# Kernel optimization log

Hardware: AMD Instinct MI355X
Metric: run time of the kernel (lower is better)

The kernel has to match this reference:

```python
import jax, jax.numpy as jnp
import numpy as np

N_USERS = 60000
N_ITEMS = 40000
N_NODES = N_USERS + N_ITEMS
N_EDGES = 1_000_000
D = 64
BN_EPS = 1e-3  # tf.layers.batch_normalization default epsilon


def setup_inputs() -> dict:
    key = jax.random.key(0)
    ks = jax.random.split(key, 16)
    s = 1.0 / np.sqrt(D)  # uniform-ish init scale for [D,D] weights
    w = lambda k: (jax.random.uniform(k, (D, D), jnp.float32, -1.0, 1.0) * s)
    return {
        "u_features": jax.random.normal(ks[0], (N_USERS, D), jnp.float32),
        "v_features": jax.random.normal(ks[1], (N_ITEMS, D), jnp.float32),
        "edge_start": jax.random.randint(ks[2], (N_EDGES,), 0, N_NODES, jnp.int32),
        "edge_end": jax.random.randint(ks[3], (N_EDGES,), 0, N_NODES, jnp.int32),
        "Ui1": w(ks[4]), "Uj1": w(ks[5]), "Vi1": w(ks[6]), "Vj1": w(ks[7]),
        "bu1": jnp.zeros((D,), jnp.float32), "bv1": jnp.zeros((D,), jnp.float32),
        "Ui2": w(ks[8]), "Uj2": w(ks[9]), "Vi2": w(ks[10]), "Vj2": w(ks[11]),
        "bu2": jnp.zeros((D,), jnp.float32), "bv2": jnp.zeros((D,), jnp.float32),
        "R": w(ks[12]),
        "gamma1": jnp.ones((D,), jnp.float32), "beta1": jnp.zeros((D,), jnp.float32),
        "gamma2": jnp.ones((D,), jnp.float32), "beta2": jnp.zeros((D,), jnp.float32),
    }


def _stage(x, Ui, Uj, Vi, Vj, bu, bv, e_start, e_end, n_nodes):
    # gate = sigmoid(E_end@(x Vi) + E_start@(x Vj) + bv)   -> edge gather
    gate = jax.nn.sigmoid((x @ Vi)[e_end] + (x @ Vj)[e_start] + bv)  # [E, D]
    msg = gate * (x @ Ui)[e_start]                                    # [E, D]
    # x Uj + E_end.T @ msg + bu   -> scatter-add to destination nodes
    agg = jax.ops.segment_sum(msg, e_end, num_segments=n_nodes)       # [N, D]
    return x @ Uj + agg + bu


def _batchnorm(x, gamma, beta):
    mean = jnp.mean(x, axis=0)
    var = jnp.var(x, axis=0)
    return gamma * (x - mean) * jax.lax.rsqrt(var + BN_EPS) + beta


def reference(u_features, v_features, edge_start, edge_end,
              Ui1, Uj1, Vi1, Vj1, bu1, bv1,
              Ui2, Uj2, Vi2, Vj2, bu2, bv2,
              R, gamma1, beta1, gamma2, beta2):
    num_users = u_features.shape[0]
    x_in = jnp.concatenate([u_features, v_features], axis=0)  # [N, D]
    n = x_in.shape[0]
    x = _stage(x_in, Ui1, Uj1, Vi1, Vj1, bu1, bv1, edge_start, edge_end, n)
    x = jax.nn.relu(_batchnorm(x, gamma1, beta1))
    x = _stage(x, Ui2, Uj2, Vi2, Vj2, bu2, bv2, edge_start, edge_end, n)
    x = _batchnorm(x, gamma2, beta2)
    x = jax.nn.relu(x + x_in @ R)  # residual branch
    return x[:num_users], x[num_users:]
```

## Files before the change

kernel.cpp:

```cpp
#include <hip/hip_runtime.h>
#include <hip/hip_bf16.h>

#define NUSERS 60000
#define NNODES 100000
#define DD 64
#define NGB 1563
#define GMM 782
#define NBUK 196
#define ESB 2048
#define NBH 400
#define NSH 64

typedef __hip_bfloat16 bf16;
using bf16x8 = __attribute__((ext_vector_type(8))) short;
using f32x4  = __attribute__((ext_vector_type(4))) float;

__device__ __forceinline__ float b2f(bf16 x) { return __bfloat162float(x); }
__device__ __forceinline__ bf16 f2b(float x) { return __float2bfloat16(x); }
__device__ __forceinline__ unsigned short fbits(float x) {
    union { bf16 b; unsigned short u; } cv; cv.b = f2b(x); return cv.u;
}
__device__ __forceinline__ float us2f(unsigned short h) {
    union { unsigned u; float f; } t; t.u = (unsigned)h << 16; return t.f;
}
__device__ __forceinline__ float lo_bf16(unsigned w) {
    union { unsigned u; float f; } t; t.u = w << 16; return t.f;
}
__device__ __forceinline__ float hi_bf16(unsigned w) {
    union { unsigned u; float f; } t; t.u = w & 0xFFFF0000u; return t.f;
}
__device__ __forceinline__ float ldf(const void* p, size_t i, int isbf) {
    if (isbf) return b2f(((const bf16*)p)[i]);
    return ((const float*)p)[i];
}
__device__ __forceinline__ unsigned pack2(float a, float b) {
    return (unsigned)fbits(a) | ((unsigned)fbits(b) << 16);
}
__device__ __forceinline__ unsigned pr2(float x0, float x1, float a0, float a1,
                                        float b0, float b1) {
    float t0 = a0 * x0 + b0, t1 = a1 * x1 + b1;
    t0 = t0 > 0.f ? t0 : 0.f;
    t1 = t1 > 0.f ? t1 : 0.f;
    return pack2(t0, t1);
}

__global__ __launch_bounds__(256) void k_bhist(
    const int* __restrict__ ee, const unsigned short* __restrict__ hsn,
    int* __restrict__ flag, int* __restrict__ bh, int E)
{
    __shared__ int h[256];
    int t = threadIdx.x;
    if (blockIdx.x == 0) {
        int cnt = 0;
        for (int i = t; i < 1024; i += 256) {
            int e = (hsn[2 * i] >> 7) & 0xFF;
            cnt += (e >= 100 && e <= 140) ? 1 : 0;
        }
        h[t] = cnt;
        __syncthreads();
        for (int s = 128; s > 0; s >>= 1) {
            if (t < s) h[t] += h[t + s];
            __syncthreads();
        }
        if (t == 0) flag[0] = (h[0] > 512) ? 1 : 0;
        __syncthreads();
    }
    h[t] = 0;
    __syncthreads();
    for (int e = blockIdx.x * 256 + t; e < E; e += gridDim.x * 256)
        atomicAdd(&h[ee[e] >> 9], 1);
    __syncthreads();
    bh[blockIdx.x * 256 + t] = h[t];
}

__global__ __launch_bounds__(1024) void k_bscan(
    const int* __restrict__ bh, int* __restrict__ bbase,
    int* __restrict__ bcursor, float* __restrict__ redz)
{
    __shared__ int ps[1024];
    __shared__ int sd[256];
    int t = threadIdx.x;
    int col = t & 255, seg = t >> 8;
    int v = 0;
#pragma unroll 4
    for (int b = seg * 100; b < (seg + 1) * 100; b++)
        v += bh[b * 256 + col];
    ps[t] = v;
    __syncthreads();
    int vv = 0;
    if (t < 256) {
        vv = ps[t] + ps[t + 256] + ps[t + 512] + ps[t + 768];
        sd[t] = vv;
    }
    __syncthreads();
    for (int off = 1; off < 256; off <<= 1) {
        int x = (t >= off && t < 256) ? sd[t - off] : 0;
        __syncthreads();
        if (t < 256) sd[t] += x;
        __syncthreads();
    }
    if (t < 256) {
        int excl = sd[t] - vv;
        bbase[t] = excl;
        bcursor[t] = excl;
    }
    for (int i = t; i < 2 * NSH * 256; i += 1024) redz[i] = 0.f;
}

__global__ __launch_bounds__(256) void k_bscatter(
    const int* __restrict__ es, const int* __restrict__ ee,
    int* __restrict__ bcursor, unsigned* __restrict__ ebuf, int E)
{
    __shared__ int h[256], gb[256], lr[256];
    int t = threadIdx.x;
    h[t] = 0;
    lr[t] = 0;
    __syncthreads();
    int base = blockIdx.x * ESB;
    unsigned ent[8];
    int bk[8];
#pragma unroll
    for (int i = 0; i < 8; i++) {
        int e = base + t + i * 256;
        if (e < E) {
            int s = es[e], d = ee[e];
            bk[i] = d >> 9;
            ent[i] = (unsigned)s | ((unsigned)(d & 511) << 20);
            atomicAdd(&h[bk[i]], 1);
        } else bk[i] = -1;
    }
    __syncthreads();
    if (h[t]) gb[t] = atomicAdd(&bcursor[t], h[t]);
    __syncthreads();
#pragma unroll
    for (int i = 0; i < 8; i++) {
        if (bk[i] >= 0) {
            int r = atomicAdd(&lr[bk[i]], 1);
            ebuf[gb[bk[i]] + r] = ent[i];
        }
    }
}

__global__ __launch_bounds__(256) void k_group(
    const int* __restrict__ bbase, const unsigned* __restrict__ ebuf,
    int* __restrict__ rowptr, int* __restrict__ srcidx)
{
    __shared__ int h[512], sc[512];
    int b = blockIdx.x, t = threadIdx.x;
    int lo = bbase[b], hi = bbase[b + 1];
    h[t] = 0;
    h[t + 256] = 0;
    __syncthreads();
    for (int i = lo + t; i < hi; i += 256)
        atomicAdd(&h[ebuf[i] >> 20], 1);
    __syncthreads();
    sc[t] = h[t];
    sc[t + 256] = h[t + 256];
    __syncthreads();
    for (int off = 1; off < 512; off <<= 1) {
        int v0 = (t >= off) ? sc[t - off] : 0;
        int v1 = (t + 256 >= off) ? sc[t + 256 - off] : 0;
        __syncthreads();
        sc[t] += v0;
        sc[t + 256] += v1;
        __syncthreads();
    }
    int n0 = b * 512 + t, n1 = b * 512 + t + 256;
    int e0 = lo + sc[t] - h[t];
    int e1 = lo + sc[t + 256] - h[t + 256];
    if (n0 < NNODES) rowptr[n0] = e0;
    if (n1 < NNODES) rowptr[n1] = e1;
    if (b == NBUK - 1 && t == 0) rowptr[NNODES] = hi;
    h[t] = e0;
    h[t + 256] = e1;
    __syncthreads();
    for (int i = lo + t; i < hi; i += 256) {
        unsigned en = ebuf[i];
        int pos = atomicAdd(&h[en >> 20], 1);
        int s = (int)(en & 0xFFFFF);
        srcidx[pos] = s < NNODES ? s : 0;
    }
}

template <int MODE>
__device__ __forceinline__ void stage_load(
    int tile, int tid, int bfflag,
    const void* u, const void* v, const unsigned short* Aacc,
    const float* ab, uint4& w0, uint4& w1)
{
    int r = tid >> 2, c0 = (tid & 3) * 16;
    int row = tile * DD + r;
    int rowc = row < NNODES ? row : NNODES - 1;
    if (MODE == 0) {
        const void* src = (rowc < NUSERS) ? u : v;
        size_t off = (rowc < NUSERS) ? ((size_t)rowc * DD + c0)
                                     : ((size_t)(rowc - NUSERS) * DD + c0);
        if (bfflag) {
            const uint4* p = (const uint4*)((const unsigned short*)src + off);
            w0 = p[0];
            w1 = p[1];
        } else {
            const float4* p = (const float4*)((const float*)src + off);
            float4 f0 = p[0], f1 = p[1], f2 = p[2], f3 = p[3];
            w0 = make_uint4(pack2(f0.x, f0.y), pack2(f0.z, f0.w),
                            pack2(f1.x, f1.y), pack2(f1.z, f1.w));
            w1 = make_uint4(pack2(f2.x, f2.y), pack2(f2.z, f2.w),
                            pack2(f3.x, f3.y), pack2(f3.z, f3.w));
        }
    } else {
        const uint4* p = (const uint4*)(Aacc + (size_t)rowc * DD + c0);
        unsigned aw[8];
        *(uint4*)&aw[0] = p[0];
        *(uint4*)&aw[4] = p[1];
        const float4* pa = (const float4*)(ab + c0);
        const float4* pb = (const float4*)(ab + 64 + c0);
        float av[16], bv[16];
#pragma unroll
        for (int j = 0; j < 4; j++) {
            float4 fa = pa[j], fb = pb[j];
            av[4 * j] = fa.x; av[4 * j + 1] = fa.y;
            av[4 * j + 2] = fa.z; av[4 * j + 3] = fa.w;
            bv[4 * j] = fb.x; bv[4 * j + 1] = fb.y;
            bv[4 * j + 2] = fb.z; bv[4 * j + 3] = fb.w;
        }
        unsigned ow[8];
#pragma unroll
        for (int j = 0; j < 8; j++)
            ow[j] = pr2(lo_bf16(aw[j]), hi_bf16(aw[j]),
                        av[2 * j], av[2 * j + 1], bv[2 * j], bv[2 * j + 1]);
        w0 = *(uint4*)&ow[0];
        w1 = *(uint4*)&ow[4];
    }
}

__device__ __forceinline__ void stage_store(unsigned short* xbuf, int tid,
                                            const uint4& w0, const uint4& w1)
{
    int r = tid >> 2, c0 = (tid & 3) * 16;
    *(uint4*)&xbuf[r * 72 + c0] = w0;
    *((uint4*)&xbuf[r * 72 + c0] + 1) = w1;
}

template <int MODE>
__global__ __launch_bounds__(256, 4) void k_mm4_mfma(
    const void* __restrict__ u, const void* __restrict__ v,
    const float* __restrict__ red, const void* __restrict__ gm,
    const void* __restrict__ bt,
    const void* __restrict__ W0, const void* __restrict__ W1,
    const void* __restrict__ W2, const void* __restrict__ W3,
    const void* __restrict__ b0, const void* __restrict__ b1,
    const int* __restrict__ flag,
    unsigned short* __restrict__ A, unsigned short* __restrict__ Ed,
    unsigned* __restrict__ Tw)
{
    __shared__ __align__(16) unsigned short lsd[4 * DD * 72];
    __shared__ __align__(16) float abs_s[128];
    const int bfflag = flag[0];
    const int tid = threadIdx.x;

    if (MODE == 1) {
        if (tid < 64) {
            float sm = 0.f, sq = 0.f;
#pragma unroll 8
            for (int s = 0; s < NSH; s++) {
                sm += red[s * 256 + tid];
                sq += red[s * 256 + 128 + tid];
            }
            float mean = sm * (1.f / NNODES);
            float var = sq * (1.f / NNODES) - mean * mean;
            float a = ldf(gm, tid, bfflag) * rsqrtf(var + 1e-3f);
            abs_s[tid] = a;
            abs_s[64 + tid] = ldf(bt, tid, bfflag) - mean * a;
        }
        __syncthreads();
    }

    int t = blockIdx.x;
    uint4 xa, xb;
    stage_load<MODE>(t, tid, bfflag, u, v, A, abs_s, xa, xb);

    if (bfflag) {
#define WSTG_BF(m, src)                                                   \
        _Pragma("unroll")                                                 \
        for (int j = 0; j < 2; j++) {                                     \
            int i = tid + j * 256; int e0 = i * 8;                        \
            *(uint4*)&lsd[(m) * 4608 + (e0 >> 6) * 72 + (e0 & 63)] =      \
                ((const uint4*)(src))[i];                                 \
        }
        WSTG_BF(0, W0) WSTG_BF(1, W1) WSTG_BF(2, W2) WSTG_BF(3, W3)
    } else {
#define WSTG_F32(m, src)                                                  \
        _Pragma("unroll")                                                 \
        for (int j = 0; j < 4; j++) {                                     \
            int i = tid + j * 256; int e0 = i * 4;                        \
            float4 f = ((const float4*)(src))[i];                         \
            *(uint2*)&lsd[(m) * 4608 + (e0 >> 6) * 72 + (e0 & 63)] =      \
                make_uint2(pack2(f.x, f.y), pack2(f.z, f.w));             \
        }
        WSTG_F32(0, W0) WSTG_F32(1, W1) WSTG_F32(2, W2) WSTG_F32(3, W3)
    }
    __syncthreads();

    const int wv = tid >> 6, lane = tid & 63;
    const int quad = lane >> 4, ln = lane & 15;
    const int mA = (wv < 2) ? wv : 2;
    bf16x8 bfrA[2][4], bfrB[2][4];
#pragma unroll
    for (int ks = 0; ks < 2; ks++)
#pragma unroll
        for (int nt = 0; nt < 4; nt++)
#pragma unroll
            for (int j = 0; j < 8; j++)
                bfrA[ks][nt][j] = (short)lsd[mA * 4608 +
                    (ks * 32 + quad * 8 + j) * 72 + nt * 16 + ln];
    if (wv >= 2) {
#pragma unroll
        for (int ks = 0; ks < 2; ks++)
#pragma unroll
            for (int nt = 0; nt < 4; nt++)
#pragma unroll
                for (int j = 0; j < 8; j++)
                    bfrB[ks][nt][j] = (short)lsd[3 * 4608 +
                        (ks * 32 + quad * 8 + j) * 72 + nt * 16 + ln];
    }
    float bias[4];
#pragma unroll
    for (int nt = 0; nt < 4; nt++)
        bias[nt] = (wv == 0) ? ldf(b0, nt * 16 + ln, bfflag)
                 : (wv == 1) ? ldf(b1, nt * 16 + ln, bfflag) : 0.f;
    __syncthreads();

    auto compute = [&](const unsigned short* xt, int row0) {
        if (wv < 2) {
            unsigned short* stg = lsd + (2 + wv) * 4608;
#pragma unroll
            for (int rt = 0; rt < 4; rt++) {
                int m = rt * 16 + ln;
                bf16x8 af0 = *(const bf16x8*)&xt[m * 72 + quad * 8];
                bf16x8 af1 = *(const bf16x8*)&xt[m * 72 + 32 + quad * 8];
#pragma unroll
                for (int nt = 0; nt < 4; nt++) {
                    f32x4 c = {0.f, 0.f, 0.f, 0.f};
                    c = __builtin_amdgcn_mfma_f32_16x16x32_bf16(af0, bfrA[0][nt], c, 0, 0, 0);
                    c = __builtin_amdgcn_mfma_f32_16x16x32_bf16(af1, bfrA[1][nt], c, 0, 0, 0);
#pragma unroll
                    for (int r = 0; r < 4; r++) {
                        int lr = rt * 16 + quad * 4 + r;
                        float vv = c[r] + bias[nt];
                        stg[lr * 72 + nt * 16 + ln] =
                            (wv == 0) ? fbits(vv) : fbits(__expf(-vv));
                    }
                }
            }
            unsigned short* dst = (wv == 0) ? A : Ed;
            int r8 = lane >> 3, c8 = lane & 7;
#pragma unroll
            for (int p = 0; p < 8; p++) {
                int lr = p * 8 + r8;
                uint4 vv = *(const uint4*)&stg[lr * 72 + c8 * 8];
                int row = row0 + lr;
                if (row < NNODES)
                    *(uint4*)&dst[(size_t)row * DD + c8 * 8] = vv;
            }
        } else {
            const int rtb = (wv - 2) * 2;
#pragma unroll
            for (int rr = 0; rr < 2; rr++) {
                int rt = rtb + rr;
                int m = rt * 16 + ln;
                bf16x8 af0 = *(const bf16x8*)&xt[m * 72 + quad * 8];
                bf16x8 af1 = *(const bf16x8*)&xt[m * 72 + 32 + quad * 8];
#pragma unroll
                for (int nt = 0; nt < 4; nt++) {
                    f32x4 c2 = {0.f, 0.f, 0.f, 0.f};
                    f32x4 c3 = {0.f, 0.f, 0.f, 0.f};
                    c2 = __builtin_amdgcn_mfma_f32_16x16x32_bf16(af0, bfrA[0][nt], c2, 0, 0, 0);
                    c2 = __builtin_amdgcn_mfma_f32_16x16x32_bf16(af1, bfrA[1][nt], c2, 0, 0, 0);
                    c3 = __builtin_amdgcn_mfma_f32_16x16x32_bf16(af0, bfrB[0][nt], c3, 0, 0, 0);
                    c3 = __builtin_amdgcn_mfma_f32_16x16x32_bf16(af1, bfrB[1][nt], c3, 0, 0, 0);
                    int col = nt * 16 + ln;
#pragma unroll
                    for (int r = 0; r < 4; r++) {
                        int row = row0 + rt * 16 + quad * 4 + r;
                        if (row < NNODES)
                            Tw[(size_t)row * DD + col] =
                                pack2(c2[r], __expf(-c3[r]));
                    }
                }
            }
        }
    };

    stage_store(lsd, tid, xa, xb);
    int tn = t + GMM;
    if (tn < NGB)
        stage_load<MODE>(tn, tid, bfflag, u, v, A, abs_s, xa, xb);
    __syncthreads();
    int buf = 0;
    while (true) {
        compute(lsd + buf * 4608, t * DD);
        if (tn >= NGB) break;
        t = tn;
        tn += GMM;
        stage_store(lsd + (buf ^ 1) * 4608, tid, xa, xb);
        if (tn < NGB)
            stage_load<MODE>(tn, tid, bfflag, u, v, A, abs_s, xa, xb);
        __syncthreads();
        buf ^= 1;
    }
}

__global__ __launch_bounds__(256) void k_final_mfma(
    const unsigned short* __restrict__ A, const float* __restrict__ red,
    const void* __restrict__ gm, const void* __restrict__ bt,
    const void* __restrict__ u, const void* __restrict__ v,
    const void* __restrict__ R, const int* __restrict__ flag,
    void* __restrict__ out)
{
    __shared__ __align__(16) unsigned short Wls[DD][72];
    __shared__ __align__(16) unsigned short xls[DD][72];
    __shared__ __align__(16) float abf[128];
    const int bfflag = flag[0];
    const int tid = threadIdx.x;
    if (tid < 64) {
        float sm = 0.f, sq = 0.f;
#pragma unroll 8
        for (int s = 0; s < NSH; s++) {
            sm += red[s * 256 + tid];
            sq += red[s * 256 + 128 + tid];
        }
        float mean = sm * (1.f / NNODES);
        float var = sq * (1.f / NNODES) - mean * mean;
        float a = ldf(gm, tid, bfflag) * rsqrtf(var + 1e-3f);
        abf[tid] = a;
        abf[64 + tid] = ldf(bt, tid, bfflag) - mean * a;
    }
    if (bfflag) {
        for (int i = tid; i < 512; i += 256) {
            int e0 = i * 8;
            *(uint4*)&Wls[e0 >> 6][e0 & 63] = ((const uint4*)R)[i];
        }
    } else {
        for (int i = tid; i < 1024; i += 256) {
            int e0 = i * 4;
            float4 f = ((const float4*)R)[i];
            *(uint2*)&Wls[e0 >> 6][e0 & 63] =
                make_uint2(pack2(f.x, f.y), pack2(f.z, f.w));
        }
    }
    uint4 w0, w1;
    stage_load<0>(blockIdx.x, tid, bfflag, u, v, nullptr, nullptr, w0, w1);
    stage_store(&xls[0][0], tid, w0, w1);
    __syncthreads();

    const int row0 = blockIdx.x * DD;
    const int wv = tid >> 6, lane = tid & 63;
    const int quad = lane >> 4, ln = lane & 15;
    bf16x8 bfr[2][4];
#pragma unroll
    for (int ks = 0; ks < 2; ks++)
#pragma unroll
        for (int nt = 0; nt < 4; nt++)
#pragma unroll
            for (int j = 0; j < 8; j++)
                bfr[ks][nt][j] = (short)Wls[ks * 32 + quad * 8 + j][nt * 16 + ln];
    float av[4], bv[4];
#pragma unroll
    for (int nt = 0; nt < 4; nt++) {
        av[nt] = abf[nt * 16 + ln];
        bv[nt] = abf[64 + nt * 16 + ln];
    }
    const int rt = wv;
    int m = rt * 16 + ln;
    bf16x8 af0 = *(const bf16x8*)&xls[m][quad * 8];
    bf16x8 af1 = *(const bf16x8*)&xls[m][32 + quad * 8];
    __syncthreads();
#pragma unroll
    for (int nt = 0; nt < 4; nt++) {
        f32x4 c = {0.f, 0.f, 0.f, 0.f};
        c = __builtin_amdgcn_mfma_f32_16x16x32_bf16(af0, bfr[0][nt], c, 0, 0, 0);
        c = __builtin_amdgcn_mfma_f32_16x16x32_bf16(af1, bfr[1][nt], c, 0, 0, 0);
        int col = nt * 16 + ln;
#pragma unroll
        for (int r = 0; r < 4; r++) {
            int row = row0 + rt * 16 + quad * 4 + r;
            if (row < NNODES) {
                size_t o = (size_t)row * DD + col;
                float vv = av[nt] * us2f(A[o]) + bv[nt] + c[r];
                vv = vv > 0.f ? vv : 0.f;
                if (bfflag) Wls[rt * 16 + quad * 4 + r][col] = fbits(vv);
                else        ((float*)out)[o] = vv;
            }
        }
    }
    if (bfflag) {
        __syncthreads();
#pragma unroll
        for (int p = 0; p < 2; p++) {
            int ci = p * 256 + tid;
            int lr = ci >> 3, c8 = ci & 7;
            int row = row0 + lr;
            uint4 vv = *(const uint4*)&Wls[lr][c8 * 8];
            if (row < NNODES)
                *(uint4*)&((unsigned short*)out)[(size_t)row * DD + c8 * 8] = vv;
        }
    }
}

__global__ __launch_bounds__(256) void k_accum(
    const int* __restrict__ rowptr, const int* __restrict__ srcidx,
    const unsigned* __restrict__ T, const bf16* __restrict__ Ed,
    unsigned short* __restrict__ A, float* __restrict__ red)
{
    __shared__ float s1[256], s2[256];
    const int wv = threadIdx.x >> 6, c = threadIdx.x & 63;
    const int d0 = blockIdx.x * 16 + wv * 4;
    int rp0 = rowptr[d0], rp1 = rowptr[d0 + 1], rp2 = rowptr[d0 + 2],
        rp3 = rowptr[d0 + 3], rp4 = rowptr[d0 + 4];
    size_t o0 = (size_t)d0 * DD + c;
    float edA = b2f(Ed[o0]),       edB = b2f(Ed[o0 + 64]),
          edC = b2f(Ed[o0 + 128]), edD = b2f(Ed[o0 + 192]);
    float sA = us2f(A[o0]),       sB = us2f(A[o0 + 64]),
          sC = us2f(A[o0 + 128]), sD = us2f(A[o0 + 192]);

#define EDGE(sv, edv, tv) sv += lo_bf16(tv) * \
    __builtin_amdgcn_rcpf(1.f + edv * hi_bf16(tv));
#define NODE_LOOP(sv, edv, r0, r1)                                  \
    {                                                               \
        int i = r0;                                                 \
        for (; i + 7 < r1; i += 8) {                                \
            unsigned t0 = T[(size_t)srcidx[i] * DD + c];            \
            unsigned t1 = T[(size_t)srcidx[i + 1] * DD + c];        \
            unsigned t2 = T[(size_t)srcidx[i + 2] * DD + c];        \
            unsigned t3 = T[(size_t)srcidx[i + 3] * DD + c];        \
            unsigned t4 = T[(size_t)srcidx[i + 4] * DD + c];        \
            unsigned t5 = T[(size_t)srcidx[i + 5] * DD + c];        \
            unsigned t6 = T[(size_t)srcidx[i + 6] * DD + c];        \
            unsigned t7 = T[(size_t)srcidx[i + 7] * DD + c];        \
            EDGE(sv, edv, t0) EDGE(sv, edv, t1)                     \
            EDGE(sv, edv, t2) EDGE(sv, edv, t3)                     \
            EDGE(sv, edv, t4) EDGE(sv, edv, t5)                     \
            EDGE(sv, edv, t6) EDGE(sv, edv, t7)                     \
        }                                                           \
        for (; i + 3 < r1; i += 4) {                                \
            unsigned t0 = T[(size_t)srcidx[i] * DD + c];            \
            unsigned t1 = T[(size_t)srcidx[i + 1] * DD + c];        \
            unsigned t2 = T[(size_t)srcidx[i + 2] * DD + c];        \
            unsigned t3 = T[(size_t)srcidx[i + 3] * DD + c];        \
            EDGE(sv, edv, t0) EDGE(sv, edv, t1)                     \
            EDGE(sv, edv, t2) EDGE(sv, edv, t3)                     \
        }                                                           \
        for (; i < r1; i++) {                                       \
            unsigned t0 = T[(size_t)srcidx[i] * DD + c];            \
            EDGE(sv, edv, t0)                                       \
        }                                                           \
    }

    NODE_LOOP(sA, edA, rp0, rp1)
    A[o0] = fbits(sA);
    NODE_LOOP(sB, edB, rp1, rp2)
    A[o0 + 64] = fbits(sB);
    NODE_LOOP(sC, edC, rp2, rp3)
    A[o0 + 128] = fbits(sC);
    NODE_LOOP(sD, edD, rp3, rp4)
    A[o0 + 192] = fbits(sD);
#undef NODE_LOOP
#undef EDGE

    s1[threadIdx.x] = (sA + sB) + (sC + sD);
    s2[threadIdx.x] = (sA * sA + sB * sB) + (sC * sC + sD * sD);
    __syncthreads();
    if (threadIdx.x < 64) {
        float a = s1[c] + s1[64 + c] + s1[128 + c] + s1[192 + c];
        float b = s2[c] + s2[64 + c] + s2[128 + c] + s2[192 + c];
        float* sh = red + (blockIdx.x & (NSH - 1)) * 256;
        unsafeAtomicAdd(&sh[c], a);
        unsafeAtomicAdd(&sh[128 + c], b);
    }
}

extern "C" void kernel_launch(void* const* d_in, const int* in_sizes, int n_in,
                              void* d_out, int out_size, void* d_ws, size_t ws_size,
                              hipStream_t stream)
{
    const void* u   = d_in[0];
    const void* v   = d_in[1];
    const int* es   = (const int*)d_in[2];
    const int* ee   = (const int*)d_in[3];
    const void* Ui1 = d_in[4];
    const void* Uj1 = d_in[5];
    const void* Vi1 = d_in[6];
    const void* Vj1 = d_in[7];
    const void* bu1 = d_in[8];
    const void* bv1 = d_in[9];
    const void* Ui2 = d_in[10];
    const void* Uj2 = d_in[11];
    const void* Vi2 = d_in[12];
    const void* Vj2 = d_in[13];
    const void* bu2 = d_in[14];
    const void* bv2 = d_in[15];
    const void* R   = d_in[16];
    const void* g1  = d_in[17];
    const void* be1 = d_in[18];
    const void* g2  = d_in[19];
    const void* be2 = d_in[20];
    const int E = in_sizes[2];

    char* ws = (char*)d_ws;
    unsigned short* A = (unsigned short*)(ws);
    unsigned* T    = (unsigned*)(ws + 25600000);
    unsigned* ebuf = (unsigned*)(ws + 25600000);
    int* srcidx    = (int*)(ws + 51200000);
    int* bh        = (int*)(ws + 51200000);
    float* redsh   = (float*)(ws + 55200000);
    int* rowptr    = (int*)(ws + 56000000);
    int* flag      = (int*)(ws + 56804224);
    int* bbase     = (int*)(ws + 56805376);
    int* bcursor   = (int*)(ws + 56806400);
    float* red1 = redsh;
    float* red2 = redsh + NSH * 256;
    bf16* Ed = (bf16*)d_out;

    k_bhist<<<NBH, 256, 0, stream>>>(ee, (const unsigned short*)u, flag, bh, E);
    k_bscan<<<1, 1024, 0, stream>>>(bh, bbase, bcursor, redsh);
    k_bscatter<<<(E + ESB - 1) / ESB, 256, 0, stream>>>(es, ee, bcursor, ebuf, E);
    k_group<<<NBUK, 256, 0, stream>>>(bbase, ebuf, rowptr, srcidx);

    k_mm4_mfma<0><<<GMM, 256, 0, stream>>>(u, v, nullptr, nullptr, nullptr,
                                           Uj1, Vi1, Ui1, Vj1, bu1, bv1, flag,
                                           A, (unsigned short*)Ed, T);
    k_accum<<<NNODES / 16, 256, 0, stream>>>(rowptr, srcidx, T, Ed, A, red1);

    k_mm4_mfma<1><<<GMM, 256, 0, stream>>>(nullptr, nullptr, red1, g1, be1,
                                           Uj2, Vi2, Ui2, Vj2, bu2, bv2, flag,
                                           A, (unsigned short*)Ed, T);
    k_accum<<<NNODES / 16, 256, 0, stream>>>(rowptr, srcidx, T, Ed, A, red2);

    k_final_mfma<<<NGB, 256, 0, stream>>>(A, red2, g2, be2, u, v, R, flag, d_out);
}
```

Before: 335.2 us.

## Precompute per-block bucket offsets in scan; pair node loops in accumulation

The histogram now runs one block per scatter chunk, and the scan kernel emits a per-block, per-bucket base offset. The scatter kernel can then write directly without a shared histogram pass or global atomic cursor. The single-block scan now serially walks about 489 block rows with 256 threads, which may lengthen that kernel. Separately, the accumulation kernel interleaves two destination nodes' edge loops, four edges each, to raise memory-level parallelism, replacing the eight-wide unroll.

```diff
diff --git a/kernel.cpp b/kernel.cpp
--- a/kernel.cpp
+++ b/kernel.cpp
@@ -8,7 +8,6 @@
 #define GMM 782
 #define NBUK 196
 #define ESB 2048
-#define NBH 400
 #define NSH 64
 
 typedef __hip_bfloat16 bf16;
@@ -67,76 +66,59 @@
     }
     h[t] = 0;
     __syncthreads();
-    for (int e = blockIdx.x * 256 + t; e < E; e += gridDim.x * 256)
-        atomicAdd(&h[ee[e] >> 9], 1);
+    int base = blockIdx.x * ESB;
+#pragma unroll
+    for (int i = 0; i < 8; i++) {
+        int e = base + t + i * 256;
+        if (e < E) atomicAdd(&h[ee[e] >> 9], 1);
+    }
     __syncthreads();
     bh[blockIdx.x * 256 + t] = h[t];
 }
 
-__global__ __launch_bounds__(1024) void k_bscan(
+__global__ __launch_bounds__(256) void k_bscan(
     const int* __restrict__ bh, int* __restrict__ bbase,
-    int* __restrict__ bcursor, float* __restrict__ redz)
-{
-    __shared__ int ps[1024];
+    int* __restrict__ gb, float* __restrict__ redz, int nbb)
+{
     __shared__ int sd[256];
     int t = threadIdx.x;
-    int col = t & 255, seg = t >> 8;
     int v = 0;
-#pragma unroll 4
-    for (int b = seg * 100; b < (seg + 1) * 100; b++)
-        v += bh[b * 256 + col];
-    ps[t] = v;
-    __syncthreads();
-    int vv = 0;
-    if (t < 256) {
-        vv = ps[t] + ps[t + 256] + ps[t + 512] + ps[t + 768];
-        sd[t] = vv;
-    }
+    for (int b = 0; b < nbb; b++) v += bh[b * 256 + t];
+    sd[t] = v;
     __syncthreads();
     for (int off = 1; off < 256; off <<= 1) {
-        int x = (t >= off && t < 256) ? sd[t - off] : 0;
-        __syncthreads();
-        if (t < 256) sd[t] += x;
-        __syncthreads();
-    }
-    if (t < 256) {
-        int excl = sd[t] - vv;
-        bbase[t] = excl;
-        bcursor[t] = excl;
-    }
-    for (int i = t; i < 2 * NSH * 256; i += 1024) redz[i] = 0.f;
+        int x = (t >= off) ? sd[t - off] : 0;
+        __syncthreads();
+        sd[t] += x;
+        __syncthreads();
+    }
+    int run = sd[t] - v;
+    bbase[t] = run;
+    for (int b = 0; b < nbb; b++) {
+        gb[b * 256 + t] = run;
+        run += bh[b * 256 + t];
+    }
+    for (int i = t; i < 2 * NSH * 256; i += 256) redz[i] = 0.f;
 }
 
 __global__ __launch_bounds__(256) void k_bscatter(
     const int* __restrict__ es, const int* __restrict__ ee,
-    int* __restrict__ bcursor, unsigned* __restrict__ ebuf, int E)
-{
-    __shared__ int h[256], gb[256], lr[256];
+    const int* __restrict__ gb, unsigned* __restrict__ ebuf, int E)
+{
+    __shared__ int gbl[256], lr[256];
     int t = threadIdx.x;
-    h[t] = 0;
     lr[t] = 0;
+    gbl[t] = gb[blockIdx.x * 256 + t];
     __syncthreads();
     int base = blockIdx.x * ESB;
-    unsigned ent[8];
-    int bk[8];
 #pragma unroll
     for (int i = 0; i < 8; i++) {
         int e = base + t + i * 256;
         if (e < E) {
             int s = es[e], d = ee[e];
-            bk[i] = d >> 9;
-            ent[i] = (unsigned)s | ((unsigned)(d & 511) << 20);
-            atomicAdd(&h[bk[i]], 1);
-        } else bk[i] = -1;
-    }
-    __syncthreads();
-    if (h[t]) gb[t] = atomicAdd(&bcursor[t], h[t]);
-    __syncthreads();
-#pragma unroll
-    for (int i = 0; i < 8; i++) {
-        if (bk[i] >= 0) {
-            int r = atomicAdd(&lr[bk[i]], 1);
-            ebuf[gb[bk[i]] + r] = ent[i];
+            int bk = d >> 9;
+            int r = atomicAdd(&lr[bk], 1);
+            ebuf[gbl[bk] + r] = (unsigned)s | ((unsigned)(d & 511) << 20);
         }
     }
 }
@@ -525,23 +507,8 @@
 
 #define EDGE(sv, edv, tv) sv += lo_bf16(tv) * \
     __builtin_amdgcn_rcpf(1.f + edv * hi_bf16(tv));
-#define NODE_LOOP(sv, edv, r0, r1)                                  \
+#define NODE_TAIL(sv, edv, i, r1)                                   \
     {                                                               \
-        int i = r0;                                                 \
-        for (; i + 7 < r1; i += 8) {                                \
-            unsigned t0 = T[(size_t)srcidx[i] * DD + c];            \
-            unsigned t1 = T[(size_t)srcidx[i + 1] * DD + c];        \
-            unsigned t2 = T[(size_t)srcidx[i + 2] * DD + c];        \
-            unsigned t3 = T[(size_t)srcidx[i + 3] * DD + c];        \
-            unsigned t4 = T[(size_t)srcidx[i + 4] * DD + c];        \
-            unsigned t5 = T[(size_t)srcidx[i + 5] * DD + c];        \
-            unsigned t6 = T[(size_t)srcidx[i + 6] * DD + c];        \
-            unsigned t7 = T[(size_t)srcidx[i + 7] * DD + c];        \
-            EDGE(sv, edv, t0) EDGE(sv, edv, t1)                     \
-            EDGE(sv, edv, t2) EDGE(sv, edv, t3)                     \
-            EDGE(sv, edv, t4) EDGE(sv, edv, t5)                     \
-            EDGE(sv, edv, t6) EDGE(sv, edv, t7)                     \
-        }                                                           \
         for (; i + 3 < r1; i += 4) {                                \
             unsigned t0 = T[(size_t)srcidx[i] * DD + c];            \
             unsigned t1 = T[(size_t)srcidx[i + 1] * DD + c];        \
@@ -555,16 +522,36 @@
             EDGE(sv, edv, t0)                                       \
         }                                                           \
     }
-
-    NODE_LOOP(sA, edA, rp0, rp1)
+#define PAIR_LOOP(sX, edX, x0, x1, sY, edY, y0, y1)                 \
+    {                                                               \
+        int iX = x0, iY = y0;                                       \
+        while (iX + 3 < x1 && iY + 3 < y1) {                        \
+            unsigned a0 = T[(size_t)srcidx[iX] * DD + c];           \
+            unsigned a1 = T[(size_t)srcidx[iX + 1] * DD + c];       \
+            unsigned a2 = T[(size_t)srcidx[iX + 2] * DD + c];       \
+            unsigned a3 = T[(size_t)srcidx[iX + 3] * DD + c];       \
+            unsigned b0 = T[(size_t)srcidx[iY] * DD + c];           \
+            unsigned b1 = T[(size_t)srcidx[iY + 1] * DD + c];       \
+            unsigned b2 = T[(size_t)srcidx[iY + 2] * DD + c];       \
+            unsigned b3 = T[(size_t)srcidx[iY + 3] * DD + c];       \
+            EDGE(sX, edX, a0) EDGE(sX, edX, a1)                     \
+            EDGE(sX, edX, a2) EDGE(sX, edX, a3)                     \
+            EDGE(sY, edY, b0) EDGE(sY, edY, b1)                     \
+            EDGE(sY, edY, b2) EDGE(sY, edY, b3)                     \
+            iX += 4; iY += 4;                                       \
+        }                                                           \
+        NODE_TAIL(sX, edX, iX, x1)                                  \
+        NODE_TAIL(sY, edY, iY, y1)                                  \
+    }
+
+    PAIR_LOOP(sA, edA, rp0, rp1, sB, edB, rp1, rp2)
     A[o0] = fbits(sA);
-    NODE_LOOP(sB, edB, rp1, rp2)
     A[o0 + 64] = fbits(sB);
-    NODE_LOOP(sC, edC, rp2, rp3)
+    PAIR_LOOP(sC, edC, rp2, rp3, sD, edD, rp3, rp4)
     A[o0 + 128] = fbits(sC);
-    NODE_LOOP(sD, edD, rp3, rp4)
     A[o0 + 192] = fbits(sD);
-#undef NODE_LOOP
+#undef PAIR_LOOP
+#undef NODE_TAIL
 #undef EDGE
 
     s1[threadIdx.x] = (sA + sB) + (sC + sD);
@@ -605,6 +592,7 @@
     const void* g2  = d_in[19];
     const void* be2 = d_in[20];
     const int E = in_sizes[2];
+    const int NBB = (E + ESB - 1) / ESB;
 
     char* ws = (char*)d_ws;
     unsigned short* A = (unsigned short*)(ws);
@@ -612,18 +600,18 @@
     unsigned* ebuf = (unsigned*)(ws + 25600000);
     int* srcidx    = (int*)(ws + 51200000);
     int* bh        = (int*)(ws + 51200000);
+    int* gb        = (int*)(ws + 53200000);
     float* redsh   = (float*)(ws + 55200000);
     int* rowptr    = (int*)(ws + 56000000);
     int* flag      = (int*)(ws + 56804224);
     int* bbase     = (int*)(ws + 56805376);
-    int* bcursor   = (int*)(ws + 56806400);
     float* red1 = redsh;
     float* red2 = redsh + NSH * 256;
     bf16* Ed = (bf16*)d_out;
 
-    k_bhist<<<NBH, 256, 0, stream>>>(ee, (const unsigned short*)u, flag, bh, E);
-    k_bscan<<<1, 1024, 0, stream>>>(bh, bbase, bcursor, redsh);
-    k_bscatter<<<(E + ESB - 1) / ESB, 256, 0, stream>>>(es, ee, bcursor, ebuf, E);
+    k_bhist<<<NBB, 256, 0, stream>>>(ee, (const unsigned short*)u, flag, bh, E);
+    k_bscan<<<1, 256, 0, stream>>>(bh, bbase, gb, redsh, NBB);
+    k_bscatter<<<NBB, 256, 0, stream>>>(es, ee, gb, ebuf, E);
     k_group<<<NBUK, 256, 0, stream>>>(bbase, ebuf, rowptr, srcidx);
 
     k_mm4_mfma<0><<<GMM, 256, 0, stream>>>(u, v, nullptr, nullptr, nullptr,
```

Result: slower. 429.6 us (+28.2%).
